# Performance work log

Measured on AMD Instinct MI355X. Metric: run time of the kernel, lower is better.

Reference implementation:

```python
import jax, jax.numpy as jnp
import numpy as np

MEM_SLOTS, NUM_HEADS, HEAD_SIZE, KEY_SIZE = 8, 8, 128, 128
MEM_SIZE = NUM_HEADS * HEAD_SIZE  # 1024
NUM_GATES = 2 * MEM_SIZE          # 2048 (gate_style='unit')
B, T, INPUT_SIZE = 128, 32, 1024


def _ln(x, g, b, eps=1e-5):
    m = x.mean(-1, keepdims=True)
    v = ((x - m) ** 2).mean(-1, keepdims=True)
    return (x - m) / jnp.sqrt(v + eps) * g + b


def setup_inputs() -> dict:
    key = jax.random.key(0)
    ks = jax.random.split(key, 12)
    s = 0.02  # weight init scale
    memory = jnp.tile(jnp.eye(MEM_SLOTS, MEM_SIZE, dtype=jnp.float32)[None], (B, 1, 1))
    return {
        'x': jax.random.normal(ks[0], (B, T, INPUT_SIZE), jnp.float32),
        'memory': memory,
        'Wi': s * jax.random.normal(ks[1], (INPUT_SIZE, MEM_SIZE), jnp.float32),
        'bi': jnp.zeros((MEM_SIZE,), jnp.float32),
        'Wq': s * jax.random.normal(ks[2], (MEM_SIZE, KEY_SIZE * NUM_HEADS), jnp.float32),
        'bq': jnp.zeros((KEY_SIZE * NUM_HEADS,), jnp.float32),
        'Wk': s * jax.random.normal(ks[3], (MEM_SIZE, KEY_SIZE * NUM_HEADS), jnp.float32),
        'bk': jnp.zeros((KEY_SIZE * NUM_HEADS,), jnp.float32),
        'Wv': s * jax.random.normal(ks[4], (MEM_SIZE, HEAD_SIZE * NUM_HEADS), jnp.float32),
        'bv': jnp.zeros((HEAD_SIZE * NUM_HEADS,), jnp.float32),
        'Wm': s * jax.random.normal(ks[5], (MEM_SIZE, MEM_SIZE), jnp.float32),
        'bm': jnp.zeros((MEM_SIZE,), jnp.float32),
        'ln1_g': jnp.ones((MEM_SIZE,), jnp.float32),
        'ln1_b': jnp.zeros((MEM_SIZE,), jnp.float32),
        'ln2_g': jnp.ones((MEM_SIZE,), jnp.float32),
        'ln2_b': jnp.zeros((MEM_SIZE,), jnp.float32),
        'rep_w': jax.random.normal(ks[6], (MEM_SIZE,), jnp.float32),
        'Wg': s * jax.random.normal(ks[7], (MEM_SIZE, NUM_GATES), jnp.float32),
        'bg': jnp.zeros((NUM_GATES,), jnp.float32),
        'Wmg': 0.01 * jax.random.normal(ks[8], (MEM_SLOTS, MEM_SIZE, NUM_GATES), jnp.float32),
        'forget_bias': jnp.asarray(1.0, jnp.float32),
        'input_bias': jnp.asarray(0.0, jnp.float32),
    }


def reference(x, memory, Wi, bi, Wq, bq, Wk, bk, Wv, bv, Wm, bm,
              ln1_g, ln1_b, ln2_g, ln2_b, rep_w, Wg, bg, Wmg,
              forget_bias, input_bias):
    Bx, S, D, H, K = x.shape[0], MEM_SLOTS, MEM_SIZE, NUM_HEADS, KEY_SIZE

    def step(mem, xt):                             # mem: (B,S,D), xt: (B,input)
        inp = xt @ Wi + bi                         # input_projector -> (B,D)
        inp_r = inp[:, None, :]                    # (B,1,D)
        # --- multihead attention: q from memory, k/v from projected input ---
        q = (mem @ Wq + bq).reshape(Bx, S, H, K).transpose(0, 2, 1, 3)   # (B,H,S,K)
        k = (inp_r @ Wk + bk).reshape(Bx, 1, H, K).transpose(0, 2, 1, 3)  # (B,H,1,K)
        v = (inp_r @ Wv + bv).reshape(Bx, 1, H, HEAD_SIZE).transpose(0, 2, 1, 3)
        scores = jax.nn.softmax(jnp.einsum('bhsk,bhtk->bhst', q, k), axis=-1)  # unscaled, per source
        att = jnp.einsum('bhst,bhtd->bhsd', scores, v)
        att = att.transpose(0, 2, 1, 3).reshape(Bx, S, D)
        # --- residual + LN, shared-weight 2-layer relu MLP, residual + LN ---
        m1 = _ln(mem + att, ln1_g, ln1_b)
        h = jax.nn.relu(m1 @ Wm + bm)
        h = jax.nn.relu(h @ Wm + bm)               # ModuleList([l]*2) shares weights
        m2 = _ln(m1 + h, ln2_g, ln2_b)
        # --- gates (computed from OLD memory and projected input) ---
        gi = (jax.nn.relu(rep_w * inp_r).mean(axis=1) @ Wg + bg)[:, None, :]  # RepeatLinear
        gm = jnp.einsum('bsd,sdg->bsg', jnp.tanh(mem), Wmg)                    # GroupLinearLayer
        gates = gm + gi                                                        # (B,S,2D)
        ig, fg = jnp.split(gates, 2, axis=-1)
        ig = jax.nn.sigmoid(ig + input_bias)
        fg = jax.nn.sigmoid(fg + forget_bias)
        new_mem = ig * jnp.tanh(m2) + fg * mem
        return new_mem, new_mem.reshape(Bx, S * D)

    final_mem, outs = jax.lax.scan(step, memory, x.transpose(1, 0, 2))
    return outs, final_mem  # outs: (T,B,S*D)
```

## Files before the change

### kernel.cpp

```cpp
#include <hip/hip_runtime.h>
#include <math.h>

#define DMEM   1024
#define NGATES 2048
#define NB     128
#define NT     32

__device__ inline float sigm(float x) { return 1.f / (1.f + __expf(-x)); }

__global__ __launch_bounds__(256)
void gemm128(const float* __restrict__ A, int lda,
             const float* __restrict__ W, int N,
             const float* __restrict__ bias,
             float* __restrict__ C, int K)
{
    __shared__ float As[16][132];
    __shared__ float Bs[16][132];
    const int tid  = threadIdx.x;
    const int tr   = (tid >> 4) << 2;
    const int tc   = (tid & 15) << 2;
    const int row0 = blockIdx.y * 128, col0 = blockIdx.x * 128;
    const int arow = tid >> 1, ah = (tid & 1) * 8;
    const int brow = tid >> 4, bcol = (tid & 15) * 8;

    float acc[8][8] = {};

    for (int k0 = 0; k0 < K; k0 += 16) {
        const float* ap = A + (long)(row0 + arow) * lda + k0 + ah;
        float4 a0 = *(const float4*)ap;
        float4 a1 = *(const float4*)(ap + 4);
        const float* bp = W + (long)(k0 + brow) * N + col0 + bcol;
        float4 b0 = *(const float4*)bp;
        float4 b1 = *(const float4*)(bp + 4);
        __syncthreads();
        As[ah + 0][arow] = a0.x; As[ah + 1][arow] = a0.y;
        As[ah + 2][arow] = a0.z; As[ah + 3][arow] = a0.w;
        As[ah + 4][arow] = a1.x; As[ah + 5][arow] = a1.y;
        As[ah + 6][arow] = a1.z; As[ah + 7][arow] = a1.w;
        *(float4*)&Bs[brow][bcol]     = b0;
        *(float4*)&Bs[brow][bcol + 4] = b1;
        __syncthreads();
#pragma unroll
        for (int kk = 0; kk < 16; ++kk) {
            float a[8], b[8];
            *(float4*)&a[0] = *(const float4*)&As[kk][tr];
            *(float4*)&a[4] = *(const float4*)&As[kk][64 + tr];
            *(float4*)&b[0] = *(const float4*)&Bs[kk][tc];
            *(float4*)&b[4] = *(const float4*)&Bs[kk][64 + tc];
#pragma unroll
            for (int i = 0; i < 8; ++i)
#pragma unroll
                for (int j = 0; j < 8; ++j)
                    acc[i][j] = fmaf(a[i], b[j], acc[i][j]);
        }
    }

#pragma unroll
    for (int jh = 0; jh < 2; ++jh) {
        int cbase = col0 + jh * 64 + tc;
        float4 bv = make_float4(0.f, 0.f, 0.f, 0.f);
        if (bias) bv = *(const float4*)&bias[cbase];
#pragma unroll
        for (int ih = 0; ih < 2; ++ih) {
#pragma unroll
            for (int i = 0; i < 4; ++i) {
                int row = row0 + ih * 64 + tr + i;
                float4 o = make_float4(acc[ih*4+i][jh*4+0] + bv.x,
                                       acc[ih*4+i][jh*4+1] + bv.y,
                                       acc[ih*4+i][jh*4+2] + bv.z,
                                       acc[ih*4+i][jh*4+3] + bv.w);
                *(float4*)(C + (long)row * N + cbase) = o;
            }
        }
    }
}

template<int AMODE, int ZMODE>
__global__ __launch_bounds__(256)
void gemm64(const float* __restrict__ A, int lda, long zsA, long pstride,
            const float* __restrict__ abias,
            const float* __restrict__ W, int N, long zsW,
            float* __restrict__ C, int ldc, long zsC,
            int K)
{
    __shared__ float As[32][68];
    __shared__ float Bs[32][68];
    const int tid = threadIdx.x;
    const int z   = blockIdx.z;
    int kbeg = 0, kend = K;
    if (ZMODE == 1) { int kc = K >> 1; kbeg = z * kc; kend = kbeg + kc; C += (long)z * zsC; }
    if (ZMODE == 2) { A += (long)z * zsA; W += (long)z * zsW; C += (long)z * zsC; }

    const int row0 = blockIdx.y * 64, col0 = blockIdx.x * 64;
    const int tr = (tid >> 4) << 2, tc = (tid & 15) << 2;
    const int arow = tid >> 2, aseg = (tid & 3) * 8;
    const int brow = tid >> 3, bcol = (tid & 7) * 8;

    float acc[4][4] = {};

    for (int k0 = kbeg; k0 < kend; k0 += 32) {
        float4 a0, a1;
        if (AMODE == 0) {
            const float* ap = A + (long)(row0 + arow) * lda + k0 + aseg;
            a0 = *(const float4*)ap;
            a1 = *(const float4*)(ap + 4);
        } else {
            const float* p0 = A + (long)(row0 + arow) * lda + k0 + aseg;
            const float* p1 = p0 + pstride;
            float4 q0 = *(const float4*)p0, q1 = *(const float4*)(p0 + 4);
            float4 r0 = *(const float4*)p1, r1 = *(const float4*)(p1 + 4);
            float4 c0 = *(const float4*)(abias + k0 + aseg);
            float4 c1 = *(const float4*)(abias + k0 + aseg + 4);
            a0.x = fmaxf(q0.x + r0.x + c0.x, 0.f);
            a0.y = fmaxf(q0.y + r0.y + c0.y, 0.f);
            a0.z = fmaxf(q0.z + r0.z + c0.z, 0.f);
            a0.w = fmaxf(q0.w + r0.w + c0.w, 0.f);
            a1.x = fmaxf(q1.x + r1.x + c1.x, 0.f);
            a1.y = fmaxf(q1.y + r1.y + c1.y, 0.f);
            a1.z = fmaxf(q1.z + r1.z + c1.z, 0.f);
            a1.w = fmaxf(q1.w + r1.w + c1.w, 0.f);
        }
        const float* bp = W + (long)(k0 + brow) * N + col0 + bcol;
        float4 b0 = *(const float4*)bp;
        float4 b1 = *(const float4*)(bp + 4);
        __syncthreads();
        As[aseg + 0][arow] = a0.x; As[aseg + 1][arow] = a0.y;
        As[aseg + 2][arow] = a0.z; As[aseg + 3][arow] = a0.w;
        As[aseg + 4][arow] = a1.x; As[aseg + 5][arow] = a1.y;
        As[aseg + 6][arow] = a1.z; As[aseg + 7][arow] = a1.w;
        *(float4*)&Bs[brow][bcol]     = b0;
        *(float4*)&Bs[brow][bcol + 4] = b1;
        __syncthreads();
#pragma unroll
        for (int kk = 0; kk < 32; ++kk) {
            float4 av = *(const float4*)&As[kk][tr];
            float4 bv = *(const float4*)&Bs[kk][tc];
            acc[0][0] = fmaf(av.x, bv.x, acc[0][0]); acc[0][1] = fmaf(av.x, bv.y, acc[0][1]);
            acc[0][2] = fmaf(av.x, bv.z, acc[0][2]); acc[0][3] = fmaf(av.x, bv.w, acc[0][3]);
            acc[1][0] = fmaf(av.y, bv.x, acc[1][0]); acc[1][1] = fmaf(av.y, bv.y, acc[1][1]);
            acc[1][2] = fmaf(av.y, bv.z, acc[1][2]); acc[1][3] = fmaf(av.y, bv.w, acc[1][3]);
            acc[2][0] = fmaf(av.z, bv.x, acc[2][0]); acc[2][1] = fmaf(av.z, bv.y, acc[2][1]);
            acc[2][2] = fmaf(av.z, bv.z, acc[2][2]); acc[2][3] = fmaf(av.z, bv.w, acc[2][3]);
            acc[3][0] = fmaf(av.w, bv.x, acc[3][0]); acc[3][1] = fmaf(av.w, bv.y, acc[3][1]);
            acc[3][2] = fmaf(av.w, bv.z, acc[3][2]); acc[3][3] = fmaf(av.w, bv.w, acc[3][3]);
        }
    }

#pragma unroll
    for (int i = 0; i < 4; ++i) {
        int row = row0 + tr + i;
        *(float4*)(C + (long)row * ldc + col0 + tc) =
            make_float4(acc[i][0], acc[i][1], acc[i][2], acc[i][3]);
    }
}

__device__ inline void block_reduce2(float& s1, float& s2)
{
    __shared__ float red[2][4];
#pragma unroll
    for (int off = 32; off > 0; off >>= 1) {
        s1 += __shfl_down(s1, off, 64);
        s2 += __shfl_down(s2, off, 64);
    }
    int tid = threadIdx.x;
    if ((tid & 63) == 0) { red[0][tid >> 6] = s1; red[1][tid >> 6] = s2; }
    __syncthreads();
    s1 = red[0][0] + red[0][1] + red[0][2] + red[0][3];
    s2 = red[1][0] + red[1][1] + red[1][2] + red[1][3];
}

__global__ __launch_bounds__(256)
void ln1_kern(const float* __restrict__ memprev, const float* __restrict__ v,
              const float* __restrict__ g, const float* __restrict__ bb,
              float* __restrict__ m1, float* __restrict__ tm)
{
    const int row = blockIdx.x;
    const int b   = row >> 3;
    const int d   = threadIdx.x << 2;

    float4 mv = *(const float4*)(memprev + (long)row * DMEM + d);
    float4 vv = *(const float4*)(v + ((long)b * NT) * DMEM + d);

    float4 tmo = make_float4(tanhf(mv.x), tanhf(mv.y), tanhf(mv.z), tanhf(mv.w));
    *(float4*)(tm + (long)row * DMEM + d) = tmo;

    float x0 = mv.x + vv.x, x1 = mv.y + vv.y, x2 = mv.z + vv.z, x3 = mv.w + vv.w;
    float s1 = x0 + x1 + x2 + x3;
    float s2 = x0 * x0 + x1 * x1 + x2 * x2 + x3 * x3;
    block_reduce2(s1, s2);
    float mean = s1 * (1.f / 1024.f);
    float var  = s2 * (1.f / 1024.f) - mean * mean;
    float inv  = 1.f / sqrtf(var + 1e-5f);

    float4 gg = *(const float4*)&g[d];
    float4 bv = *(const float4*)&bb[d];
    *(float4*)(m1 + (long)row * DMEM + d) =
        make_float4((x0 - mean) * inv * gg.x + bv.x,
                    (x1 - mean) * inv * gg.y + bv.y,
                    (x2 - mean) * inv * gg.z + bv.z,
                    (x3 - mean) * inv * gg.w + bv.w);
}

__global__ __launch_bounds__(256)
void ln2_kern(float* m1io, const float* __restrict__ P,
              const float* __restrict__ bm,
              const float* __restrict__ g, const float* __restrict__ bb)
{
    const int row = blockIdx.x;
    const int d   = threadIdx.x << 2;
    const long o  = (long)row * DMEM + d;

    float4 a  = *(const float4*)(m1io + o);
    float4 p0 = *(const float4*)(P + o);
    float4 p1 = *(const float4*)(P + 1048576 + o);
    float4 bv = *(const float4*)&bm[d];
    float h0 = fmaxf(p0.x + p1.x + bv.x, 0.f);
    float h1 = fmaxf(p0.y + p1.y + bv.y, 0.f);
    float h2 = fmaxf(p0.z + p1.z + bv.z, 0.f);
    float h3 = fmaxf(p0.w + p1.w + bv.w, 0.f);
    float x0 = a.x + h0, x1 = a.y + h1, x2 = a.z + h2, x3 = a.w + h3;

    float s1 = x0 + x1 + x2 + x3;
    float s2 = x0 * x0 + x1 * x1 + x2 * x2 + x3 * x3;
    block_reduce2(s1, s2);
    float mean = s1 * (1.f / 1024.f);
    float var  = s2 * (1.f / 1024.f) - mean * mean;
    float inv  = 1.f / sqrtf(var + 1e-5f);

    float4 gg = *(const float4*)&g[d];
    float4 b2 = *(const float4*)&bb[d];
    *(float4*)(m1io + o) =
        make_float4(tanhf((x0 - mean) * inv * gg.x + b2.x),
                    tanhf((x1 - mean) * inv * gg.y + b2.y),
                    tanhf((x2 - mean) * inv * gg.z + b2.z),
                    tanhf((x3 - mean) * inv * gg.w + b2.w));
}

__global__ __launch_bounds__(256)
void gate_ln1_kern(const float* __restrict__ gm, const float* __restrict__ gi,
                   int t, const float* t2, const float* __restrict__ memprev,
                   const float* __restrict__ fbp, const float* __restrict__ ibp,
                   const float* __restrict__ v,
                   const float* __restrict__ g, const float* __restrict__ bb,
                   float* __restrict__ outp, float* m1, float* __restrict__ tm,
                   int last)
{
    const int row = blockIdx.x;
    const int b   = row >> 3;
    const int d   = threadIdx.x << 2;
    const float ib = *ibp;
    const float fb = *fbp;

    float4 g0 = *(const float4*)(gm + (long)row * NGATES + d);
    float4 g1 = *(const float4*)(gm + (long)row * NGATES + DMEM + d);
    float4 i0 = *(const float4*)(gi + ((long)b * NT + t) * NGATES + d);
    float4 i1 = *(const float4*)(gi + ((long)b * NT + t) * NGATES + DMEM + d);
    float4 tv = *(const float4*)(t2 + (long)row * DMEM + d);
    float4 mv = *(const float4*)(memprev + (long)row * DMEM + d);

    float4 o;
    o.x = sigm(g0.x + i0.x + ib) * tv.x + sigm(g1.x + i1.x + fb) * mv.x;
    o.y = sigm(g0.y + i0.y + ib) * tv.y + sigm(g1.y + i1.y + fb) * mv.y;
    o.z = sigm(g0.z + i0.z + ib) * tv.z + sigm(g1.z + i1.z + fb) * mv.z;
    o.w = sigm(g0.w + i0.w + ib) * tv.w + sigm(g1.w + i1.w + fb) * mv.w;
    *(float4*)(outp + (long)row * DMEM + d) = o;

    if (!last) {
        float4 vv = *(const float4*)(v + ((long)b * NT + t + 1) * DMEM + d);
        *(float4*)(tm + (long)row * DMEM + d) =
            make_float4(tanhf(o.x), tanhf(o.y), tanhf(o.z), tanhf(o.w));

        float x0 = o.x + vv.x, x1 = o.y + vv.y, x2 = o.z + vv.z, x3 = o.w + vv.w;
        float s1 = x0 + x1 + x2 + x3;
        float s2 = x0 * x0 + x1 * x1 + x2 * x2 + x3 * x3;
        block_reduce2(s1, s2);
        float mean = s1 * (1.f / 1024.f);
        float var  = s2 * (1.f / 1024.f) - mean * mean;
        float inv  = 1.f / sqrtf(var + 1e-5f);

        float4 gg = *(const float4*)&g[d];
        float4 bv = *(const float4*)&bb[d];
        *(float4*)(m1 + (long)row * DMEM + d) =
            make_float4((x0 - mean) * inv * gg.x + bv.x,
                        (x1 - mean) * inv * gg.y + bv.y,
                        (x2 - mean) * inv * gg.z + bv.z,
                        (x3 - mean) * inv * gg.w + bv.w);
    }
}

__global__ __launch_bounds__(256)
void ga_kern(float* __restrict__ inp, const float* __restrict__ rep)
{
    long i4 = ((long)blockIdx.x * 256 + threadIdx.x) << 2;
    float4 x = *(const float4*)&inp[i4];
    float4 r = *(const float4*)&rep[i4 & (DMEM - 1)];
    *(float4*)&inp[i4] = make_float4(fmaxf(r.x * x.x, 0.f), fmaxf(r.y * x.y, 0.f),
                                     fmaxf(r.z * x.z, 0.f), fmaxf(r.w * x.w, 0.f));
}

extern "C" void kernel_launch(void* const* d_in, const int* in_sizes, int n_in,
                              void* d_out, int out_size, void* d_ws, size_t ws_size,
                              hipStream_t stream)
{
    const float* x    = (const float*)d_in[0];
    const float* mem0 = (const float*)d_in[1];
    const float* Wi   = (const float*)d_in[2];
    const float* bi   = (const float*)d_in[3];
    const float* Wv   = (const float*)d_in[8];
    const float* bv   = (const float*)d_in[9];
    const float* Wm   = (const float*)d_in[10];
    const float* bm   = (const float*)d_in[11];
    const float* ln1g = (const float*)d_in[12];
    const float* ln1b = (const float*)d_in[13];
    const float* ln2g = (const float*)d_in[14];
    const float* ln2b = (const float*)d_in[15];
    const float* repw = (const float*)d_in[16];
    const float* Wg   = (const float*)d_in[17];
    const float* bg   = (const float*)d_in[18];
    const float* Wmg  = (const float*)d_in[19];
    const float* fbp  = (const float*)d_in[20];
    const float* ibp  = (const float*)d_in[21];

    float* out = (float*)d_out;
    char*  ws  = (char*)d_ws;
    const long MB = 1024L * 1024L;

    float* v    = (float*)(ws + 0 * MB);
    float* gi   = (float*)(ws + 16 * MB);
    float* m1   = (float*)(ws + 48 * MB);
    float* tm   = (float*)(ws + 52 * MB);
    float* hP   = (float*)(ws + 56 * MB);
    float* gm   = (float*)(ws + 64 * MB);
    float* h2P  = (float*)(ws + 72 * MB);
    float* inp  = (float*)(ws + 48 * MB);

    dim3 blk(256);

    gemm128<<<dim3(8, 32, 1), blk, 0, stream>>>(x, 1024, Wi, 1024, bi, inp, 1024);
    gemm128<<<dim3(8, 32, 1), blk, 0, stream>>>(inp, 1024, Wv, 1024, bv, v, 1024);
    ga_kern<<<4096, blk, 0, stream>>>(inp, repw);
    gemm128<<<dim3(16, 32, 1), blk, 0, stream>>>(inp, 1024, Wg, 2048, bg, gi, 1024);

    ln1_kern<<<1024, blk, 0, stream>>>(mem0, v, ln1g, ln1b, m1, tm);

    const long stepN = (long)NB * 8 * DMEM;
    for (int t = 0; t < NT; ++t) {
        const float* memprev = (t == 0) ? mem0 : out + (long)(t - 1) * stepN;

        gemm64<0, 2><<<dim3(32, 2, 8), blk, 0, stream>>>(
            tm, 8192, 1024, 0, nullptr, Wmg, 2048, 2097152, gm, 16384, 2048, 1024);
        gemm64<0, 1><<<dim3(16, 16, 2), blk, 0, stream>>>(
            m1, 1024, 0, 0, nullptr, Wm, 1024, 0, hP, 1024, 1048576, 1024);
        gemm64<1, 1><<<dim3(16, 16, 2), blk, 0, stream>>>(
            hP, 1024, 0, 1048576, bm, Wm, 1024, 0, h2P, 1024, 1048576, 1024);
        ln2_kern<<<1024, blk, 0, stream>>>(m1, h2P, bm, ln2g, ln2b);
        gate_ln1_kern<<<1024, blk, 0, stream>>>(
            gm, gi, t, m1, memprev, fbp, ibp, v, ln1g, ln1b,
            out + (long)t * stepN, m1, tm, (t == NT - 1) ? 1 : 0);
    }

    hipMemcpyAsync(out + 32L * stepN, out + 31L * stepN, stepN * sizeof(float),
                   hipMemcpyDeviceToDevice, stream);
}
```

Baseline: 5.434 ms.

## Unify GEMMs into double-buffered 128-row tile kernel and fuse LN2 with gating

Replaces the separate 128x128 and 64x64 GEMM kernels with one templated GEMM. It uses 128-row tiles, a 32-deep K step, LDS double buffering with register prefetch, and optional split-K. The per-slot memory-gate GEMM now uses split-K with 128-row tiles, and the LN2 kernel is merged into the gate/LN1 kernel, so each step launches four kernels instead of five. The gate partial sums share workspace with the MLP hidden partials, and the fused kernel now reduces the split-K partials. This trades fewer, larger blocks and more LDS for less launch overhead and better operand reuse.

```diff
diff --git a/kernel.cpp b/kernel.cpp
--- a/kernel.cpp
+++ b/kernel.cpp
@@ -8,155 +8,130 @@
 
 __device__ inline float sigm(float x) { return 1.f / (1.f + __expf(-x)); }
 
+template<int BN, int AMODE, int SPLITK, bool BIAS>
 __global__ __launch_bounds__(256)
-void gemm128(const float* __restrict__ A, int lda,
-             const float* __restrict__ W, int N,
-             const float* __restrict__ bias,
-             float* __restrict__ C, int K)
-{
-    __shared__ float As[16][132];
-    __shared__ float Bs[16][132];
+void gemm_d(const float* __restrict__ A, int lda, long zsA, long psA,
+            const float* __restrict__ abias,
+            const float* __restrict__ W, int ldw, long zsW,
+            const float* __restrict__ bias,
+            float* __restrict__ C, int ldc, long zsC, long psC,
+            int K)
+{
+    __shared__ float As[2][32][132];
+    __shared__ float Bs[2][32][BN + 4];
+
     const int tid  = threadIdx.x;
-    const int tr   = (tid >> 4) << 2;
-    const int tc   = (tid & 15) << 2;
-    const int row0 = blockIdx.y * 128, col0 = blockIdx.x * 128;
-    const int arow = tid >> 1, ah = (tid & 1) * 8;
-    const int brow = tid >> 4, bcol = (tid & 15) * 8;
-
-    float acc[8][8] = {};
-
-    for (int k0 = 0; k0 < K; k0 += 16) {
+    const int slot = blockIdx.z / SPLITK;
+    const int kc   = blockIdx.z % SPLITK;
+    A += (long)slot * zsA;
+    W += (long)slot * zsW;
+    C += (long)slot * zsC + (long)kc * psC;
+    const int kchunk = K / SPLITK;
+    const int kbeg   = kc * kchunk;
+    const int NIT    = kchunk / 32;
+
+    const int row0 = blockIdx.y * 128;
+    const int col0 = blockIdx.x * BN;
+
+    const int arow = tid >> 1;
+    const int ah   = (tid & 1) * 16;
+    const int bkr  = tid >> 3;
+    const int bc   = (tid & 7) * (BN / 8);
+    const int tr = (tid >> 4) << 2;
+    const int tc = (tid & 15) << 2;
+
+    float4 a_st[4];
+    float4 b_st[BN / 32];
+
+    auto load_regs = [&](int k0) {
         const float* ap = A + (long)(row0 + arow) * lda + k0 + ah;
-        float4 a0 = *(const float4*)ap;
-        float4 a1 = *(const float4*)(ap + 4);
-        const float* bp = W + (long)(k0 + brow) * N + col0 + bcol;
-        float4 b0 = *(const float4*)bp;
-        float4 b1 = *(const float4*)(bp + 4);
-        __syncthreads();
-        As[ah + 0][arow] = a0.x; As[ah + 1][arow] = a0.y;
-        As[ah + 2][arow] = a0.z; As[ah + 3][arow] = a0.w;
-        As[ah + 4][arow] = a1.x; As[ah + 5][arow] = a1.y;
-        As[ah + 6][arow] = a1.z; As[ah + 7][arow] = a1.w;
-        *(float4*)&Bs[brow][bcol]     = b0;
-        *(float4*)&Bs[brow][bcol + 4] = b1;
-        __syncthreads();
-#pragma unroll
-        for (int kk = 0; kk < 16; ++kk) {
-            float a[8], b[8];
-            *(float4*)&a[0] = *(const float4*)&As[kk][tr];
-            *(float4*)&a[4] = *(const float4*)&As[kk][64 + tr];
-            *(float4*)&b[0] = *(const float4*)&Bs[kk][tc];
-            *(float4*)&b[4] = *(const float4*)&Bs[kk][64 + tc];
+#pragma unroll
+        for (int j = 0; j < 4; ++j) {
+            if (AMODE == 0) {
+                a_st[j] = *(const float4*)(ap + j * 4);
+            } else {
+                float4 p0 = *(const float4*)(ap + j * 4);
+                float4 p1 = *(const float4*)(ap + psA + j * 4);
+                float4 bb = *(const float4*)(abias + k0 + ah + j * 4);
+                a_st[j].x = fmaxf(p0.x + p1.x + bb.x, 0.f);
+                a_st[j].y = fmaxf(p0.y + p1.y + bb.y, 0.f);
+                a_st[j].z = fmaxf(p0.z + p1.z + bb.z, 0.f);
+                a_st[j].w = fmaxf(p0.w + p1.w + bb.w, 0.f);
+            }
+        }
+        const float* wp = W + (long)(k0 + bkr) * ldw + col0 + bc;
+#pragma unroll
+        for (int j = 0; j < BN / 32; ++j)
+            b_st[j] = *(const float4*)(wp + j * 4);
+    };
+
+    auto write_lds = [&](int p) {
+#pragma unroll
+        for (int j = 0; j < 4; ++j) {
+            As[p][ah + j * 4 + 0][arow] = a_st[j].x;
+            As[p][ah + j * 4 + 1][arow] = a_st[j].y;
+            As[p][ah + j * 4 + 2][arow] = a_st[j].z;
+            As[p][ah + j * 4 + 3][arow] = a_st[j].w;
+        }
+#pragma unroll
+        for (int j = 0; j < BN / 32; ++j)
+            *(float4*)&Bs[p][bkr][bc + j * 4] = b_st[j];
+    };
+
+    float acc[8][BN / 16] = {};
+
+    auto compute = [&](int p) {
+#pragma unroll
+        for (int kk = 0; kk < 32; ++kk) {
+            float a[8], b[BN / 16];
+            *(float4*)&a[0] = *(const float4*)&As[p][kk][tr];
+            *(float4*)&a[4] = *(const float4*)&As[p][kk][64 + tr];
+            *(float4*)&b[0] = *(const float4*)&Bs[p][kk][tc];
+            if (BN == 128)
+                *(float4*)&b[4] = *(const float4*)&Bs[p][kk][64 + tc];
 #pragma unroll
             for (int i = 0; i < 8; ++i)
 #pragma unroll
-                for (int j = 0; j < 8; ++j)
+                for (int j = 0; j < BN / 16; ++j)
                     acc[i][j] = fmaf(a[i], b[j], acc[i][j]);
         }
-    }
-
-#pragma unroll
-    for (int jh = 0; jh < 2; ++jh) {
+    };
+
+    load_regs(kbeg);
+    write_lds(0);
+    int p = 0;
+    for (int it = 0; it < NIT; ++it) {
+        __syncthreads();
+        if (it + 1 < NIT) load_regs(kbeg + (it + 1) * 32);
+        compute(p);
+        if (it + 1 < NIT) write_lds(p ^ 1);
+        p ^= 1;
+    }
+
+#pragma unroll
+    for (int jh = 0; jh < BN / 64; ++jh) {
         int cbase = col0 + jh * 64 + tc;
         float4 bv = make_float4(0.f, 0.f, 0.f, 0.f);
-        if (bias) bv = *(const float4*)&bias[cbase];
+        if (BIAS) bv = *(const float4*)&bias[cbase];
 #pragma unroll
         for (int ih = 0; ih < 2; ++ih) {
 #pragma unroll
             for (int i = 0; i < 4; ++i) {
                 int row = row0 + ih * 64 + tr + i;
-                float4 o = make_float4(acc[ih*4+i][jh*4+0] + bv.x,
-                                       acc[ih*4+i][jh*4+1] + bv.y,
-                                       acc[ih*4+i][jh*4+2] + bv.z,
-                                       acc[ih*4+i][jh*4+3] + bv.w);
-                *(float4*)(C + (long)row * N + cbase) = o;
+                float4 o = make_float4(acc[ih * 4 + i][jh * 4 + 0] + bv.x,
+                                       acc[ih * 4 + i][jh * 4 + 1] + bv.y,
+                                       acc[ih * 4 + i][jh * 4 + 2] + bv.z,
+                                       acc[ih * 4 + i][jh * 4 + 3] + bv.w);
+                *(float4*)(C + (long)row * ldc + cbase) = o;
             }
         }
     }
 }
 
-template<int AMODE, int ZMODE>
-__global__ __launch_bounds__(256)
-void gemm64(const float* __restrict__ A, int lda, long zsA, long pstride,
-            const float* __restrict__ abias,
-            const float* __restrict__ W, int N, long zsW,
-            float* __restrict__ C, int ldc, long zsC,
-            int K)
-{
-    __shared__ float As[32][68];
-    __shared__ float Bs[32][68];
-    const int tid = threadIdx.x;
-    const int z   = blockIdx.z;
-    int kbeg = 0, kend = K;
-    if (ZMODE == 1) { int kc = K >> 1; kbeg = z * kc; kend = kbeg + kc; C += (long)z * zsC; }
-    if (ZMODE == 2) { A += (long)z * zsA; W += (long)z * zsW; C += (long)z * zsC; }
-
-    const int row0 = blockIdx.y * 64, col0 = blockIdx.x * 64;
-    const int tr = (tid >> 4) << 2, tc = (tid & 15) << 2;
-    const int arow = tid >> 2, aseg = (tid & 3) * 8;
-    const int brow = tid >> 3, bcol = (tid & 7) * 8;
-
-    float acc[4][4] = {};
-
-    for (int k0 = kbeg; k0 < kend; k0 += 32) {
-        float4 a0, a1;
-        if (AMODE == 0) {
-            const float* ap = A + (long)(row0 + arow) * lda + k0 + aseg;
-            a0 = *(const float4*)ap;
-            a1 = *(const float4*)(ap + 4);
-        } else {
-            const float* p0 = A + (long)(row0 + arow) * lda + k0 + aseg;
-            const float* p1 = p0 + pstride;
-            float4 q0 = *(const float4*)p0, q1 = *(const float4*)(p0 + 4);
-            float4 r0 = *(const float4*)p1, r1 = *(const float4*)(p1 + 4);
-            float4 c0 = *(const float4*)(abias + k0 + aseg);
-            float4 c1 = *(const float4*)(abias + k0 + aseg + 4);
-            a0.x = fmaxf(q0.x + r0.x + c0.x, 0.f);
-            a0.y = fmaxf(q0.y + r0.y + c0.y, 0.f);
-            a0.z = fmaxf(q0.z + r0.z + c0.z, 0.f);
-            a0.w = fmaxf(q0.w + r0.w + c0.w, 0.f);
-            a1.x = fmaxf(q1.x + r1.x + c1.x, 0.f);
-            a1.y = fmaxf(q1.y + r1.y + c1.y, 0.f);
-            a1.z = fmaxf(q1.z + r1.z + c1.z, 0.f);
-            a1.w = fmaxf(q1.w + r1.w + c1.w, 0.f);
-        }
-        const float* bp = W + (long)(k0 + brow) * N + col0 + bcol;
-        float4 b0 = *(const float4*)bp;
-        float4 b1 = *(const float4*)(bp + 4);
-        __syncthreads();
-        As[aseg + 0][arow] = a0.x; As[aseg + 1][arow] = a0.y;
-        As[aseg + 2][arow] = a0.z; As[aseg + 3][arow] = a0.w;
-        As[aseg + 4][arow] = a1.x; As[aseg + 5][arow] = a1.y;
-        As[aseg + 6][arow] = a1.z; As[aseg + 7][arow] = a1.w;
-        *(float4*)&Bs[brow][bcol]     = b0;
-        *(float4*)&Bs[brow][bcol + 4] = b1;
-        __syncthreads();
-#pragma unroll
-        for (int kk = 0; kk < 32; ++kk) {
-            float4 av = *(const float4*)&As[kk][tr];
-            float4 bv = *(const float4*)&Bs[kk][tc];
-            acc[0][0] = fmaf(av.x, bv.x, acc[0][0]); acc[0][1] = fmaf(av.x, bv.y, acc[0][1]);
-            acc[0][2] = fmaf(av.x, bv.z, acc[0][2]); acc[0][3] = fmaf(av.x, bv.w, acc[0][3]);
-            acc[1][0] = fmaf(av.y, bv.x, acc[1][0]); acc[1][1] = fmaf(av.y, bv.y, acc[1][1]);
-            acc[1][2] = fmaf(av.y, bv.z, acc[1][2]); acc[1][3] = fmaf(av.y, bv.w, acc[1][3]);
-            acc[2][0] = fmaf(av.z, bv.x, acc[2][0]); acc[2][1] = fmaf(av.z, bv.y, acc[2][1]);
-            acc[2][2] = fmaf(av.z, bv.z, acc[2][2]); acc[2][3] = fmaf(av.z, bv.w, acc[2][3]);
-            acc[3][0] = fmaf(av.w, bv.x, acc[3][0]); acc[3][1] = fmaf(av.w, bv.y, acc[3][1]);
-            acc[3][2] = fmaf(av.w, bv.z, acc[3][2]); acc[3][3] = fmaf(av.w, bv.w, acc[3][3]);
-        }
-    }
-
-#pragma unroll
-    for (int i = 0; i < 4; ++i) {
-        int row = row0 + tr + i;
-        *(float4*)(C + (long)row * ldc + col0 + tc) =
-            make_float4(acc[i][0], acc[i][1], acc[i][2], acc[i][3]);
-    }
-}
-
 __device__ inline void block_reduce2(float& s1, float& s2)
 {
     __shared__ float red[2][4];
+    __syncthreads();
 #pragma unroll
     for (int off = 32; off > 0; off >>= 1) {
         s1 += __shfl_down(s1, off, 64);
@@ -181,8 +156,8 @@
     float4 mv = *(const float4*)(memprev + (long)row * DMEM + d);
     float4 vv = *(const float4*)(v + ((long)b * NT) * DMEM + d);
 
-    float4 tmo = make_float4(tanhf(mv.x), tanhf(mv.y), tanhf(mv.z), tanhf(mv.w));
-    *(float4*)(tm + (long)row * DMEM + d) = tmo;
+    *(float4*)(tm + (long)row * DMEM + d) =
+        make_float4(tanhf(mv.x), tanhf(mv.y), tanhf(mv.z), tanhf(mv.w));
 
     float x0 = mv.x + vv.x, x1 = mv.y + vv.y, x2 = mv.z + vv.z, x3 = mv.w + vv.w;
     float s1 = x0 + x1 + x2 + x3;
@@ -202,23 +177,30 @@
 }
 
 __global__ __launch_bounds__(256)
-void ln2_kern(float* m1io, const float* __restrict__ P,
-              const float* __restrict__ bm,
-              const float* __restrict__ g, const float* __restrict__ bb)
+void step_fused(const float* __restrict__ m1in, const float* __restrict__ h2P,
+                const float* __restrict__ bm,
+                const float* __restrict__ g2, const float* __restrict__ b2,
+                const float* __restrict__ gmP, const float* __restrict__ gi, int t,
+                const float* __restrict__ memprev,
+                const float* __restrict__ fbp, const float* __restrict__ ibp,
+                const float* __restrict__ v,
+                const float* __restrict__ g1, const float* __restrict__ b1,
+                float* __restrict__ outp, float* __restrict__ m1out,
+                float* __restrict__ tm, int last)
 {
     const int row = blockIdx.x;
+    const int b   = row >> 3;
     const int d   = threadIdx.x << 2;
     const long o  = (long)row * DMEM + d;
 
-    float4 a  = *(const float4*)(m1io + o);
-    float4 p0 = *(const float4*)(P + o);
-    float4 p1 = *(const float4*)(P + 1048576 + o);
-    float4 bv = *(const float4*)&bm[d];
-    float h0 = fmaxf(p0.x + p1.x + bv.x, 0.f);
-    float h1 = fmaxf(p0.y + p1.y + bv.y, 0.f);
-    float h2 = fmaxf(p0.z + p1.z + bv.z, 0.f);
-    float h3 = fmaxf(p0.w + p1.w + bv.w, 0.f);
-    float x0 = a.x + h0, x1 = a.y + h1, x2 = a.z + h2, x3 = a.w + h3;
+    float4 a  = *(const float4*)(m1in + o);
+    float4 q0 = *(const float4*)(h2P + o);
+    float4 q1 = *(const float4*)(h2P + 1048576 + o);
+    float4 bb = *(const float4*)&bm[d];
+    float x0 = a.x + fmaxf(q0.x + q1.x + bb.x, 0.f);
+    float x1 = a.y + fmaxf(q0.y + q1.y + bb.y, 0.f);
+    float x2 = a.z + fmaxf(q0.z + q1.z + bb.z, 0.f);
+    float x3 = a.w + fmaxf(q0.w + q1.w + bb.w, 0.f);
 
     float s1 = x0 + x1 + x2 + x3;
     float s2 = x0 * x0 + x1 * x1 + x2 * x2 + x3 * x3;
@@ -227,64 +209,52 @@
     float var  = s2 * (1.f / 1024.f) - mean * mean;
     float inv  = 1.f / sqrtf(var + 1e-5f);
 
-    float4 gg = *(const float4*)&g[d];
-    float4 b2 = *(const float4*)&bb[d];
-    *(float4*)(m1io + o) =
-        make_float4(tanhf((x0 - mean) * inv * gg.x + b2.x),
-                    tanhf((x1 - mean) * inv * gg.y + b2.y),
-                    tanhf((x2 - mean) * inv * gg.z + b2.z),
-                    tanhf((x3 - mean) * inv * gg.w + b2.w));
-}
-
-__global__ __launch_bounds__(256)
-void gate_ln1_kern(const float* __restrict__ gm, const float* __restrict__ gi,
-                   int t, const float* t2, const float* __restrict__ memprev,
-                   const float* __restrict__ fbp, const float* __restrict__ ibp,
-                   const float* __restrict__ v,
-                   const float* __restrict__ g, const float* __restrict__ bb,
-                   float* __restrict__ outp, float* m1, float* __restrict__ tm,
-                   int last)
-{
-    const int row = blockIdx.x;
-    const int b   = row >> 3;
-    const int d   = threadIdx.x << 2;
-    const float ib = *ibp;
-    const float fb = *fbp;
-
-    float4 g0 = *(const float4*)(gm + (long)row * NGATES + d);
-    float4 g1 = *(const float4*)(gm + (long)row * NGATES + DMEM + d);
-    float4 i0 = *(const float4*)(gi + ((long)b * NT + t) * NGATES + d);
-    float4 i1 = *(const float4*)(gi + ((long)b * NT + t) * NGATES + DMEM + d);
-    float4 tv = *(const float4*)(t2 + (long)row * DMEM + d);
-    float4 mv = *(const float4*)(memprev + (long)row * DMEM + d);
-
-    float4 o;
-    o.x = sigm(g0.x + i0.x + ib) * tv.x + sigm(g1.x + i1.x + fb) * mv.x;
-    o.y = sigm(g0.y + i0.y + ib) * tv.y + sigm(g1.y + i1.y + fb) * mv.y;
-    o.z = sigm(g0.z + i0.z + ib) * tv.z + sigm(g1.z + i1.z + fb) * mv.z;
-    o.w = sigm(g0.w + i0.w + ib) * tv.w + sigm(g1.w + i1.w + fb) * mv.w;
-    *(float4*)(outp + (long)row * DMEM + d) = o;
+    float4 gg = *(const float4*)&g2[d];
+    float4 b2v = *(const float4*)&b2[d];
+    float t20 = tanhf((x0 - mean) * inv * gg.x + b2v.x);
+    float t21 = tanhf((x1 - mean) * inv * gg.y + b2v.y);
+    float t22 = tanhf((x2 - mean) * inv * gg.z + b2v.z);
+    float t23 = tanhf((x3 - mean) * inv * gg.w + b2v.w);
+
+    const float ib = *ibp, fb = *fbp;
+    const long go = (long)row * NGATES + d;
+    float4 ga0 = *(const float4*)(gmP + go);
+    float4 ga1 = *(const float4*)(gmP + 2097152 + go);
+    float4 gb0 = *(const float4*)(gmP + go + DMEM);
+    float4 gb1 = *(const float4*)(gmP + 2097152 + go + DMEM);
+    const long io = ((long)b * NT + t) * NGATES + d;
+    float4 i0 = *(const float4*)(gi + io);
+    float4 i1 = *(const float4*)(gi + io + DMEM);
+    float4 mv = *(const float4*)(memprev + o);
+
+    float4 out;
+    out.x = sigm(ga0.x + ga1.x + i0.x + ib) * t20 + sigm(gb0.x + gb1.x + i1.x + fb) * mv.x;
+    out.y = sigm(ga0.y + ga1.y + i0.y + ib) * t21 + sigm(gb0.y + gb1.y + i1.y + fb) * mv.y;
+    out.z = sigm(ga0.z + ga1.z + i0.z + ib) * t22 + sigm(gb0.z + gb1.z + i1.z + fb) * mv.z;
+    out.w = sigm(ga0.w + ga1.w + i0.w + ib) * t23 + sigm(gb0.w + gb1.w + i1.w + fb) * mv.w;
+    *(float4*)(outp + o) = out;
 
     if (!last) {
         float4 vv = *(const float4*)(v + ((long)b * NT + t + 1) * DMEM + d);
-        *(float4*)(tm + (long)row * DMEM + d) =
-            make_float4(tanhf(o.x), tanhf(o.y), tanhf(o.z), tanhf(o.w));
-
-        float x0 = o.x + vv.x, x1 = o.y + vv.y, x2 = o.z + vv.z, x3 = o.w + vv.w;
-        float s1 = x0 + x1 + x2 + x3;
-        float s2 = x0 * x0 + x1 * x1 + x2 * x2 + x3 * x3;
-        block_reduce2(s1, s2);
-        float mean = s1 * (1.f / 1024.f);
-        float var  = s2 * (1.f / 1024.f) - mean * mean;
-        float inv  = 1.f / sqrtf(var + 1e-5f);
-
-        float4 gg = *(const float4*)&g[d];
-        float4 bv = *(const float4*)&bb[d];
-        *(float4*)(m1 + (long)row * DMEM + d) =
-            make_float4((x0 - mean) * inv * gg.x + bv.x,
-                        (x1 - mean) * inv * gg.y + bv.y,
-                        (x2 - mean) * inv * gg.z + bv.z,
-                        (x3 - mean) * inv * gg.w + bv.w);
+        *(float4*)(tm + o) =
+            make_float4(tanhf(out.x), tanhf(out.y), tanhf(out.z), tanhf(out.w));
+
+        float y0 = out.x + vv.x, y1 = out.y + vv.y;
+        float y2 = out.z + vv.z, y3 = out.w + vv.w;
+        float u1 = y0 + y1 + y2 + y3;
+        float u2 = y0 * y0 + y1 * y1 + y2 * y2 + y3 * y3;
+        block_reduce2(u1, u2);
+        float mean1 = u1 * (1.f / 1024.f);
+        float var1  = u2 * (1.f / 1024.f) - mean1 * mean1;
+        float inv1  = 1.f / sqrtf(var1 + 1e-5f);
+
+        float4 g1v = *(const float4*)&g1[d];
+        float4 b1v = *(const float4*)&b1[d];
+        *(float4*)(m1out + o) =
+            make_float4((y0 - mean1) * inv1 * g1v.x + b1v.x,
+                        (y1 - mean1) * inv1 * g1v.y + b1v.y,
+                        (y2 - mean1) * inv1 * g1v.z + b1v.z,
+                        (y3 - mean1) * inv1 * g1v.w + b1v.w);
     }
 }
 
@@ -329,17 +299,20 @@
     float* gi   = (float*)(ws + 16 * MB);
     float* m1   = (float*)(ws + 48 * MB);
     float* tm   = (float*)(ws + 52 * MB);
+    float* gmP  = (float*)(ws + 56 * MB);
     float* hP   = (float*)(ws + 56 * MB);
-    float* gm   = (float*)(ws + 64 * MB);
     float* h2P  = (float*)(ws + 72 * MB);
     float* inp  = (float*)(ws + 48 * MB);
 
     dim3 blk(256);
 
-    gemm128<<<dim3(8, 32, 1), blk, 0, stream>>>(x, 1024, Wi, 1024, bi, inp, 1024);
-    gemm128<<<dim3(8, 32, 1), blk, 0, stream>>>(inp, 1024, Wv, 1024, bv, v, 1024);
+    gemm_d<128, 0, 1, true><<<dim3(8, 32, 1), blk, 0, stream>>>(
+        x, 1024, 0, 0, nullptr, Wi, 1024, 0, bi, inp, 1024, 0, 0, 1024);
+    gemm_d<128, 0, 1, true><<<dim3(8, 32, 1), blk, 0, stream>>>(
+        inp, 1024, 0, 0, nullptr, Wv, 1024, 0, bv, v, 1024, 0, 0, 1024);
     ga_kern<<<4096, blk, 0, stream>>>(inp, repw);
-    gemm128<<<dim3(16, 32, 1), blk, 0, stream>>>(inp, 1024, Wg, 2048, bg, gi, 1024);
+    gemm_d<128, 0, 1, true><<<dim3(16, 32, 1), blk, 0, stream>>>(
+        inp, 1024, 0, 0, nullptr, Wg, 2048, 0, bg, gi, 2048, 0, 0, 1024);
 
     ln1_kern<<<1024, blk, 0, stream>>>(mem0, v, ln1g, ln1b, m1, tm);
 
@@ -347,16 +320,19 @@
     for (int t = 0; t < NT; ++t) {
         const float* memprev = (t == 0) ? mem0 : out + (long)(t - 1) * stepN;
 
-        gemm64<0, 2><<<dim3(32, 2, 8), blk, 0, stream>>>(
-            tm, 8192, 1024, 0, nullptr, Wmg, 2048, 2097152, gm, 16384, 2048, 1024);
-        gemm64<0, 1><<<dim3(16, 16, 2), blk, 0, stream>>>(
-            m1, 1024, 0, 0, nullptr, Wm, 1024, 0, hP, 1024, 1048576, 1024);
-        gemm64<1, 1><<<dim3(16, 16, 2), blk, 0, stream>>>(
-            hP, 1024, 0, 1048576, bm, Wm, 1024, 0, h2P, 1024, 1048576, 1024);
-        ln2_kern<<<1024, blk, 0, stream>>>(m1, h2P, bm, ln2g, ln2b);
-        gate_ln1_kern<<<1024, blk, 0, stream>>>(
-            gm, gi, t, m1, memprev, fbp, ibp, v, ln1g, ln1b,
-            out + (long)t * stepN, m1, tm, (t == NT - 1) ? 1 : 0);
+        gemm_d<64, 0, 2, false><<<dim3(16, 8, 2), blk, 0, stream>>>(
+            m1, 1024, 0, 0, nullptr, Wm, 1024, 0, nullptr,
+            hP, 1024, 0, 1048576, 1024);
+        gemm_d<64, 1, 2, false><<<dim3(16, 8, 2), blk, 0, stream>>>(
+            hP, 1024, 0, 1048576, bm, Wm, 1024, 0, nullptr,
+            h2P, 1024, 0, 1048576, 1024);
+        gemm_d<128, 0, 2, false><<<dim3(16, 1, 16), blk, 0, stream>>>(
+            tm, 8192, 1024, 0, nullptr, Wmg, 2048, 2097152, nullptr,
+            gmP, 16384, 2048, 2097152, 1024);
+        step_fused<<<1024, blk, 0, stream>>>(
+            m1, h2P, bm, ln2g, ln2b, gmP, gi, t, memprev, fbp, ibp,
+            v, ln1g, ln1b, out + (long)t * stepN, m1, tm,
+            (t == NT - 1) ? 1 : 0);
     }
 
     hipMemcpyAsync(out + 32L * stepN, out + 31L * stepN, stepN * sizeof(float),
```

New measurement: 15.75 ms. 2.9x slower.
